# Optimization experiments

Measured on AMD Instinct MI355X. Metric: run time of the kernel, lower is better.

Reference implementation:

```python
import jax, jax.numpy as jnp
import numpy as np

T, D, FF, E, R = 4096, 1024, 2048, 4, 16
LORA_SCALE = 32.0 / 16.0  # alpha / r


def setup_inputs() -> dict:
    key = jax.random.key(0)
    ks = jax.random.split(key, 12)
    return {
        "x": jax.random.normal(ks[0], (T, D), jnp.float32),
        "gate_w": jax.random.normal(ks[1], (E, D), jnp.float32) * 0.03,
        "gate_up_w": jax.random.normal(ks[2], (D, 2 * FF), jnp.float32)[None].repeat(E, 0) * 0.0
                     + jax.random.normal(ks[2], (E, D, 2 * FF), jnp.float32) * 0.03,
        "gate_up_b": jax.random.normal(ks[3], (E, 2 * FF), jnp.float32) * 0.01,
        "down_w": jax.random.normal(ks[4], (E, FF, D), jnp.float32) * 0.02,
        "down_b": jax.random.normal(ks[5], (E, D), jnp.float32) * 0.01,
        "A_gate": jax.random.normal(ks[6], (E, R, D), jnp.float32) * 0.02,
        "B_gate": jax.random.normal(ks[7], (E, FF, R), jnp.float32) * 0.02,
        "A_up": jax.random.normal(ks[8], (E, R, D), jnp.float32) * 0.02,
        "B_up": jax.random.normal(ks[9], (E, FF, R), jnp.float32) * 0.02,
        "A_down": jax.random.normal(ks[10], (E, R, FF), jnp.float32) * 0.02,
        "B_down": jax.random.normal(ks[11], (E, D, R), jnp.float32) * 0.02,
        "top_k": 2,
    }


def reference(x, gate_w, gate_up_w, gate_up_b, down_w, down_b,
              A_gate, B_gate, A_up, B_up, A_down, B_down, top_k):
    t, d = x.shape
    e = gate_w.shape[0]
    # --- router: logits, softmax (fp32), top-k, renormalize ---
    router_logits = x @ gate_w.T                                   # [T,E]
    rw = jax.nn.softmax(router_logits.astype(jnp.float32), axis=1)
    top_w, sel = jax.lax.top_k(rw, top_k)                          # [T,k]
    top_w = top_w / jnp.sum(top_w, axis=-1, keepdims=True)
    top_w = top_w.astype(x.dtype)
    # dense per-token per-expert combine weights (scatter of top-k weights)
    w = jnp.zeros((t, e), x.dtype).at[jnp.arange(t)[:, None], sel].add(top_w)  # [T,E]
    # --- per-expert SwiGLU MLP with LoRA (vectorized over experts) ---
    gu = jnp.einsum('td,edf->etf', x, gate_up_w) + gate_up_b[:, None, :]       # [E,T,2FF]
    ff = gu.shape[-1] // 2
    gate = gu[..., :ff] + jnp.einsum('td,erd,efr->etf', x, A_gate, B_gate) * LORA_SCALE
    up = gu[..., ff:] + jnp.einsum('td,erd,efr->etf', x, A_up, B_up) * LORA_SCALE
    act = jax.nn.silu(gate) * up                                               # [E,T,FF]
    down = jnp.einsum('etf,efd->etd', act, down_w) + down_b[:, None, :]
    down = down + jnp.einsum('etf,erf,edr->etd', act, A_down, B_down) * LORA_SCALE
    # --- weighted scatter-combine ---
    final = jnp.einsum('etd,te->td', down, w)                                  # [T,D]
    return final, router_logits
```

## Files before the change

kernel.cpp:

```cpp
#include <hip/hip_runtime.h>

#define T_TOK 4096
#define DIM   1024
#define FFD   2048
#define NEXP  4
#define NRP   8704
#define MTILES 68

typedef unsigned short u16;
typedef __attribute__((ext_vector_type(8))) short short8;
typedef __attribute__((ext_vector_type(4))) float f32x4;
typedef __attribute__((ext_vector_type(8))) unsigned short u16x8;
typedef __attribute__((ext_vector_type(4))) unsigned short u16x4;

typedef __attribute__((address_space(1))) unsigned int as1_u32;
typedef __attribute__((address_space(3))) unsigned int as3_u32;

__device__ __forceinline__ u16 f2bf(float f) {
  union { float f; unsigned u; } v; v.f = f;
  unsigned u = v.u;
  return (u16)((u + 0x7fffu + ((u >> 16) & 1u)) >> 16);
}
__device__ __forceinline__ float bf2f(u16 h) {
  union { unsigned u; float f; } v; v.u = ((unsigned)h) << 16;
  return v.f;
}
__device__ __forceinline__ void gload16(const void* g, void* l) {
  __builtin_amdgcn_global_load_lds((const as1_u32*)g, (as3_u32*)l, 16, 0, 0);
}

__global__ void router_k(const float* __restrict__ x, const float* __restrict__ gw,
                         float* __restrict__ logits_out, int* __restrict__ sel,
                         float* __restrict__ selw) {
  int t = blockIdx.x;
  int lane = threadIdx.x;
  float xv[16];
#pragma unroll
  for (int i = 0; i < 16; ++i) xv[i] = x[(size_t)t * DIM + lane + i * 64];
  float l[4];
#pragma unroll
  for (int e = 0; e < 4; ++e) {
    float s = 0.f;
#pragma unroll
    for (int i = 0; i < 16; ++i) s += xv[i] * gw[e * DIM + lane + i * 64];
#pragma unroll
    for (int off = 32; off > 0; off >>= 1) s += __shfl_xor(s, off, 64);
    l[e] = s;
  }
  if (lane == 0) {
#pragma unroll
    for (int e = 0; e < 4; ++e) logits_out[(size_t)t * 4 + e] = l[e];
    int e0 = 0; float b0 = l[0];
    for (int e = 1; e < 4; ++e) if (l[e] > b0) { b0 = l[e]; e0 = e; }
    int e1 = -1; float b1 = -3.4e38f;
    for (int e = 0; e < 4; ++e) if (e != e0 && l[e] > b1) { b1 = l[e]; e1 = e; }
    float p1 = expf(b1 - b0);
    float w0 = 1.f / (1.f + p1);
    sel[2 * t] = e0; sel[2 * t + 1] = e1;
    selw[2 * t] = w0; selw[2 * t + 1] = 1.f - w0;
  }
}

__global__ void scan_k(const int* __restrict__ sel, int* __restrict__ pos,
                       int* __restrict__ offs, int* __restrict__ rowtok,
                       int* __restrict__ pairrow) {
  __shared__ int base[4];
  __shared__ int wsum[16][4];
  __shared__ int off_s[5];
  int tid = threadIdx.x, lane = tid & 63, wid = tid >> 6;
  if (tid < 4) base[tid] = 0;
  __syncthreads();
  for (int chunk = 0; chunk < 4; ++chunk) {
    int t = chunk * 1024 + tid;
    int e0 = sel[2 * t], e1 = sel[2 * t + 1];
    unsigned long long ltm = (1ull << lane) - 1ull;
    bool f[4]; int within[4];
#pragma unroll
    for (int e = 0; e < 4; ++e) {
      f[e] = (e0 == e) || (e1 == e);
      unsigned long long m = __ballot(f[e]);
      within[e] = __popcll(m & ltm);
      if (lane == 0) wsum[wid][e] = __popcll(m);
    }
    __syncthreads();
    int wbase[4] = {0, 0, 0, 0}, tot[4] = {0, 0, 0, 0};
    for (int i = 0; i < 16; ++i)
#pragma unroll
      for (int e = 0; e < 4; ++e) {
        int v = wsum[i][e];
        if (i < wid) wbase[e] += v;
        tot[e] += v;
      }
#pragma unroll
    for (int e = 0; e < 4; ++e)
      if (f[e]) {
        int p = base[e] + wbase[e] + within[e];
        if (e0 == e) pos[2 * t] = p; else pos[2 * t + 1] = p;
      }
    __syncthreads();
    if (tid < 4) base[tid] += tot[tid];
    __syncthreads();
  }
  if (tid == 0) {
    int o = 0;
    for (int e = 0; e < 4; ++e) { off_s[e] = o; o += ((base[e] + 127) >> 7) << 7; }
    off_s[4] = o;
    for (int i = 0; i < 5; ++i) offs[i] = off_s[i];
  }
  __syncthreads();
  for (int r = tid; r < NRP; r += 1024) rowtok[r] = -1;
  __syncthreads();
  for (int t = tid; t < T_TOK; t += 1024) {
#pragma unroll
    for (int s = 0; s < 2; ++s) {
      int e = sel[2 * t + s];
      int rr = off_s[e] + pos[2 * t + s];
      pairrow[2 * t + s] = rr;
      rowtok[rr] = t;
    }
  }
}

__global__ void gather_k(const float* __restrict__ x, const int* __restrict__ rowtok,
                         u16* __restrict__ xg) {
  int r = blockIdx.x, tid = threadIdx.x;
  int t = rowtok[r];
  float4 v = make_float4(0.f, 0.f, 0.f, 0.f);
  if (t >= 0) v = ((const float4*)(x + (size_t)t * DIM))[tid];
  u16x4 o;
  o[0] = f2bf(v.x); o[1] = f2bf(v.y); o[2] = f2bf(v.z); o[3] = f2bf(v.w);
  ((u16x4*)(xg + (size_t)r * DIM))[tid] = o;
}

__global__ void cvtA_k(const float* __restrict__ Ag, const float* __restrict__ Au,
                       const float* __restrict__ Ad, u16* __restrict__ abgu,
                       u16* __restrict__ adb) {
  int g = blockIdx.x * 256 + threadIdx.x;
  if (g < 32768) {
    int flat = g * 4;
    int e = flat >> 15;
    int rem = flat & 32767;
    int q = rem >> 10;
    int d = rem & 1023;
    const float* src = (q < 16) ? (Ag + ((size_t)e * 16 + q) * DIM + d)
                                : (Au + ((size_t)e * 16 + (q - 16)) * DIM + d);
    float4 v = *(const float4*)src;
    u16x4 o; o[0] = f2bf(v.x); o[1] = f2bf(v.y); o[2] = f2bf(v.z); o[3] = f2bf(v.w);
    *(u16x4*)(abgu + (size_t)flat) = o;
  } else {
    int flat = (g - 32768) * 4;
    float4 v = *(const float4*)(Ad + flat);
    u16x4 o; o[0] = f2bf(v.x); o[1] = f2bf(v.y); o[2] = f2bf(v.z); o[3] = f2bf(v.w);
    *(u16x4*)(adb + (size_t)flat) = o;
  }
}

__global__ void xa_k(const u16* __restrict__ xg, const u16* __restrict__ abgu,
                     const int* __restrict__ offs, float* __restrict__ xagu) {
  int r0 = blockIdx.x * 2, lane = threadIdx.x;
  int e = 0;
  if (r0 >= offs[1]) e = 1;
  if (r0 >= offs[2]) e = 2;
  if (r0 >= offs[3]) e = 3;
  float x0[16], x1[16];
#pragma unroll
  for (int i = 0; i < 4; ++i) {
    u16x4 v0 = ((const u16x4*)(xg + (size_t)r0 * DIM))[lane + i * 64];
    u16x4 v1 = ((const u16x4*)(xg + (size_t)(r0 + 1) * DIM))[lane + i * 64];
#pragma unroll
    for (int j = 0; j < 4; ++j) { x0[i * 4 + j] = bf2f(v0[j]); x1[i * 4 + j] = bf2f(v1[j]); }
  }
  const u16* A = abgu + (size_t)e * 32 * DIM;
  for (int q = 0; q < 32; ++q) {
    float s0 = 0.f, s1 = 0.f;
#pragma unroll
    for (int i = 0; i < 4; ++i) {
      u16x4 av = ((const u16x4*)(A + (size_t)q * DIM))[lane + i * 64];
#pragma unroll
      for (int j = 0; j < 4; ++j) {
        float a = bf2f(av[j]);
        s0 += x0[i * 4 + j] * a; s1 += x1[i * 4 + j] * a;
      }
    }
#pragma unroll
    for (int off = 32; off > 0; off >>= 1) { s0 += __shfl_xor(s0, off, 64); s1 += __shfl_xor(s1, off, 64); }
    if (lane == 0) { xagu[(size_t)r0 * 32 + q] = s0; xagu[(size_t)(r0 + 1) * 32 + q] = s1; }
  }
}

__global__ void aad_k(const u16* __restrict__ act, const u16* __restrict__ adb,
                      const int* __restrict__ offs, float* __restrict__ aad) {
  int r0 = blockIdx.x * 2, lane = threadIdx.x;
  int e = 0;
  if (r0 >= offs[1]) e = 1;
  if (r0 >= offs[2]) e = 2;
  if (r0 >= offs[3]) e = 3;
  float x0[32], x1[32];
#pragma unroll
  for (int i = 0; i < 8; ++i) {
    u16x4 v0 = ((const u16x4*)(act + (size_t)r0 * FFD))[lane + i * 64];
    u16x4 v1 = ((const u16x4*)(act + (size_t)(r0 + 1) * FFD))[lane + i * 64];
#pragma unroll
    for (int j = 0; j < 4; ++j) { x0[i * 4 + j] = bf2f(v0[j]); x1[i * 4 + j] = bf2f(v1[j]); }
  }
  const u16* A = adb + (size_t)e * 16 * FFD;
  for (int q = 0; q < 16; ++q) {
    float s0 = 0.f, s1 = 0.f;
#pragma unroll
    for (int i = 0; i < 8; ++i) {
      u16x4 av = ((const u16x4*)(A + (size_t)q * FFD))[lane + i * 64];
#pragma unroll
      for (int j = 0; j < 4; ++j) {
        float a = bf2f(av[j]);
        s0 += x0[i * 4 + j] * a; s1 += x1[i * 4 + j] * a;
      }
    }
#pragma unroll
    for (int off = 32; off > 0; off >>= 1) { s0 += __shfl_xor(s0, off, 64); s1 += __shfl_xor(s1, off, 64); }
    if (lane == 0) { aad[(size_t)r0 * 16 + q] = s0; aad[(size_t)(r0 + 1) * 16 + q] = s1; }
  }
}

__global__ void transpose_k(const float* __restrict__ in, u16* __restrict__ out,
                            int K, int N) {
  int e = blockIdx.z;
  int n0 = blockIdx.x * 32, k0 = blockIdx.y * 32;
  const float* I = in + (size_t)e * K * N;
  u16* O = out + (size_t)e * N * K;
  __shared__ u16 tile[32][33];
#pragma unroll
  for (int i = 0; i < 4; ++i) {
    int k = k0 + threadIdx.y + i * 8;
    tile[threadIdx.y + i * 8][threadIdx.x] = f2bf(I[(size_t)k * N + n0 + threadIdx.x]);
  }
  __syncthreads();
#pragma unroll
  for (int i = 0; i < 4; ++i) {
    int n = n0 + threadIdx.y + i * 8;
    O[(size_t)n * K + k0 + threadIdx.x] = tile[threadIdx.x][threadIdx.y + i * 8];
  }
}

__global__ __launch_bounds__(256, 2) void gemm1_k(
    const u16* __restrict__ xg, const u16* __restrict__ wgu_t,
    const float* __restrict__ gub, const float* __restrict__ Bg,
    const float* __restrict__ Bu, const float* __restrict__ xagu,
    const int* __restrict__ offs, u16* __restrict__ act) {
  __shared__ __align__(16) u16 sAB[36864];
  int tid = threadIdx.x, w = tid >> 6, lane = tid & 63;
  int f0 = blockIdx.x * 128;
  int row0 = blockIdx.y * 128;
  int e = 0;
  if (row0 >= offs[1]) e = 1;
  if (row0 >= offs[2]) e = 2;
  if (row0 >= offs[3]) e = 3;
  int wm = w >> 1, wn = w & 1;

  int srow = lane >> 2;
  int scol = ((lane & 3) ^ ((lane >> 3) & 3)) * 8;
  const u16* gA = xg + (size_t)(row0 + w * 32 + srow) * DIM + scol;
  int bhalf = (w < 2) ? (f0 + w * 64) : (2048 + f0 + (w - 2) * 64);
  const u16* gB = wgu_t + ((size_t)e << 22) + (size_t)(bhalf + srow) * DIM + scol;
  int fo = (((lane >> 4) ^ ((lane >> 1) & 3))) * 8;
  int arb = (wm * 64 + (lane & 15)) * 32 + fo;
  int brb = 4096 + (wn * 128 + (lane & 15)) * 32 + fo;

  f32x4 acc[4][8];
#pragma unroll
  for (int i = 0; i < 4; ++i)
#pragma unroll
    for (int j = 0; j < 8; ++j) acc[i][j] = f32x4{0.f, 0.f, 0.f, 0.f};

#pragma unroll
  for (int p = 0; p < 2; ++p) {
    u16* dA = sAB + p * 12288 + w * 1024;
    gload16(gA + p * 32, dA); gload16(gA + 16 * DIM + p * 32, dA + 512);
    u16* dB = sAB + p * 12288 + 4096 + w * 2048;
    gload16(gB + p * 32, dB); gload16(gB + 16 * DIM + p * 32, dB + 512);
    gload16(gB + 32 * DIM + p * 32, dB + 1024); gload16(gB + 48 * DIM + p * 32, dB + 1536);
  }
#pragma unroll
  for (int t = 0; t < 32; ++t) {
    if (t == 31) asm volatile("s_waitcnt vmcnt(0)\n\ts_barrier" ::: "memory");
    else         asm volatile("s_waitcnt vmcnt(6)\n\ts_barrier" ::: "memory");
    if (t < 30) {
      int kk = (t + 2) * 32;
      int bo = ((t + 2) % 3) * 12288;
      u16* dA = sAB + bo + w * 1024;
      gload16(gA + kk, dA); gload16(gA + 16 * DIM + kk, dA + 512);
      u16* dB = sAB + bo + 4096 + w * 2048;
      gload16(gB + kk, dB); gload16(gB + 16 * DIM + kk, dB + 512);
      gload16(gB + 32 * DIM + kk, dB + 1024); gload16(gB + 48 * DIM + kk, dB + 1536);
    }
    const u16* cb = sAB + (t % 3) * 12288;
    short8 a[4], bb[8];
#pragma unroll
    for (int mi = 0; mi < 4; ++mi)
      a[mi] = *(const short8*)&cb[arb + mi * 512];
#pragma unroll
    for (int ni = 0; ni < 8; ++ni)
      bb[ni] = *(const short8*)&cb[brb + ni * 512];
#pragma unroll
    for (int mi = 0; mi < 4; ++mi)
#pragma unroll
      for (int ni = 0; ni < 8; ++ni)
        acc[mi][ni] = __builtin_amdgcn_mfma_f32_16x16x32_bf16(a[mi], bb[ni], acc[mi][ni], 0, 0, 0);
  }

  __syncthreads();
  {
    int rl = tid & 127, half = tid >> 7;
    int sw = (rl >> 1) & 3;
    int abase = half * 12288 + rl * 32;
    u16 tmp[16];
#pragma unroll
    for (int q = 0; q < 16; ++q) tmp[q] = f2bf(2.f * xagu[(size_t)(row0 + rl) * 32 + half * 16 + q]);
    *(u16x8*)&sAB[abase + (0 ^ sw) * 8] = *(u16x8*)&tmp[0];
    *(u16x8*)&sAB[abase + (1 ^ sw) * 8] = *(u16x8*)&tmp[8];
    u16 t2[8] = {0x3f80, 0, 0, 0, 0, 0, 0, 0};
    u16 t3[8] = {0, 0, 0, 0, 0, 0, 0, 0};
    *(u16x8*)&sAB[abase + (2 ^ sw) * 8] = *(u16x8*)&t2[0];
    *(u16x8*)&sAB[abase + (3 ^ sw) * 8] = *(u16x8*)&t3[0];
    int r = tid, fb = r & 127, bh = r >> 7;
    int swb = (r >> 1) & 3;
    int bbase = 4096 + r * 32;
    const float* Bsrc = bh ? Bu : Bg;
    float bias = gub[e * 4096 + (bh ? (2048 + f0 + fb) : (f0 + fb))];
    u16 tb[16];
#pragma unroll
    for (int q = 0; q < 16; ++q) tb[q] = f2bf(Bsrc[((size_t)e * FFD + f0 + fb) * 16 + q]);
    *(u16x8*)&sAB[bbase + (0 ^ swb) * 8] = *(u16x8*)&tb[0];
    *(u16x8*)&sAB[bbase + (1 ^ swb) * 8] = *(u16x8*)&tb[8];
    u16 t2b[8] = {f2bf(bias), 0, 0, 0, 0, 0, 0, 0};
    *(u16x8*)&sAB[bbase + (2 ^ swb) * 8] = *(u16x8*)&t2b[0];
    *(u16x8*)&sAB[bbase + (3 ^ swb) * 8] = *(u16x8*)&t3[0];
  }
  __syncthreads();
  {
    int aBase = wn ? 12288 : 0;
    short8 a[4], bb[8];
#pragma unroll
    for (int mi = 0; mi < 4; ++mi)
      a[mi] = *(const short8*)&sAB[aBase + arb + mi * 512];
#pragma unroll
    for (int ni = 0; ni < 8; ++ni)
      bb[ni] = *(const short8*)&sAB[brb + ni * 512];
#pragma unroll
    for (int mi = 0; mi < 4; ++mi)
#pragma unroll
      for (int ni = 0; ni < 8; ++ni)
        acc[mi][ni] = __builtin_amdgcn_mfma_f32_16x16x32_bf16(a[mi], bb[ni], acc[mi][ni], 0, 0, 0);
  }
  __syncthreads();
#pragma unroll
  for (int mi = 0; mi < 4; ++mi)
#pragma unroll
    for (int ni = 0; ni < 8; ++ni)
#pragma unroll
      for (int j = 0; j < 4; ++j) {
        int row = wm * 64 + mi * 16 + (lane >> 4) * 4 + j;
        int br = wn * 128 + ni * 16 + (lane & 15);
        int key = ((row & 3) ^ ((row >> 2) & 3)) << 4;
        sAB[row * 256 + (br ^ key)] = f2bf(acc[mi][ni][j]);
      }
  __syncthreads();
  {
    int fc = (tid & 15) * 8;
    int rb = tid >> 4;
#pragma unroll
    for (int it = 0; it < 8; ++it) {
      int row = rb + it * 16;
      int key = ((row & 3) ^ ((row >> 2) & 3)) << 4;
      u16x8 gv = *(const u16x8*)&sAB[row * 256 + (fc ^ key)];
      u16x8 uv = *(const u16x8*)&sAB[row * 256 + 128 + (fc ^ key)];
      u16x8 ov;
#pragma unroll
      for (int j = 0; j < 8; ++j) {
        float g = bf2f(gv[j]);
        float u = bf2f(uv[j]);
        float s = g / (1.f + __expf(-g));
        ov[j] = f2bf(s * u);
      }
      *(u16x8*)(act + (size_t)(row0 + row) * FFD + f0 + fc) = ov;
    }
  }
}

__global__ __launch_bounds__(256, 2) void gemm2_k(
    const u16* __restrict__ act, const u16* __restrict__ wd_t,
    const float* __restrict__ db, const float* __restrict__ Bd,
    const float* __restrict__ aad, const int* __restrict__ offs,
    u16* __restrict__ down) {
  __shared__ __align__(16) u16 sAB[36864];
  int tid = threadIdx.x, w = tid >> 6, lane = tid & 63;
  int n0 = blockIdx.x * 256;
  int row0 = blockIdx.y * 128;
  int ks = blockIdx.z;
  size_t kbase = (size_t)ks * 1024;
  int e = 0;
  if (row0 >= offs[1]) e = 1;
  if (row0 >= offs[2]) e = 2;
  if (row0 >= offs[3]) e = 3;
  int wm = w >> 1, wn = w & 1;

  int srow = lane >> 2;
  int scol = ((lane & 3) ^ ((lane >> 3) & 3)) * 8;
  const u16* gA = act + (size_t)(row0 + w * 32 + srow) * FFD + kbase + scol;
  const u16* gB = wd_t + (size_t)e * DIM * FFD + (size_t)(n0 + w * 64 + srow) * FFD + kbase + scol;
  int fo = (((lane >> 4) ^ ((lane >> 1) & 3))) * 8;
  int arb = (wm * 64 + (lane & 15)) * 32 + fo;
  int brb = 4096 + (wn * 128 + (lane & 15)) * 32 + fo;

  f32x4 acc[4][8];
#pragma unroll
  for (int i = 0; i < 4; ++i)
#pragma unroll
    for (int j = 0; j < 8; ++j) acc[i][j] = f32x4{0.f, 0.f, 0.f, 0.f};

#pragma unroll
  for (int p = 0; p < 2; ++p) {
    u16* dA = sAB + p * 12288 + w * 1024;
    gload16(gA + p * 32, dA); gload16(gA + 16 * FFD + p * 32, dA + 512);
    u16* dB = sAB + p * 12288 + 4096 + w * 2048;
    gload16(gB + p * 32, dB); gload16(gB + 16 * FFD + p * 32, dB + 512);
    gload16(gB + 32 * FFD + p * 32, dB + 1024); gload16(gB + 48 * FFD + p * 32, dB + 1536);
  }
#pragma unroll
  for (int t = 0; t < 32; ++t) {
    if (t == 31) asm volatile("s_waitcnt vmcnt(0)\n\ts_barrier" ::: "memory");
    else         asm volatile("s_waitcnt vmcnt(6)\n\ts_barrier" ::: "memory");
    if (t < 30) {
      int kk = (t + 2) * 32;
      int bo = ((t + 2) % 3) * 12288;
      u16* dA = sAB + bo + w * 1024;
      gload16(gA + kk, dA); gload16(gA + 16 * FFD + kk, dA + 512);
      u16* dB = sAB + bo + 4096 + w * 2048;
      gload16(gB + kk, dB); gload16(gB + 16 * FFD + kk, dB + 512);
      gload16(gB + 32 * FFD + kk, dB + 1024); gload16(gB + 48 * FFD + kk, dB + 1536);
    }
    const u16* cb = sAB + (t % 3) * 12288;
    short8 a[4], bb[8];
#pragma unroll
    for (int mi = 0; mi < 4; ++mi)
      a[mi] = *(const short8*)&cb[arb + mi * 512];
#pragma unroll
    for (int ni = 0; ni < 8; ++ni)
      bb[ni] = *(const short8*)&cb[brb + ni * 512];
#pragma unroll
    for (int mi = 0; mi < 4; ++mi)
#pragma unroll
      for (int ni = 0; ni < 8; ++ni)
        acc[mi][ni] = __builtin_amdgcn_mfma_f32_16x16x32_bf16(a[mi], bb[ni], acc[mi][ni], 0, 0, 0);
  }

  if (ks == 0) {
    __syncthreads();
    {
      int r = tid >> 1, kh = tid & 1;
      int sw = (r >> 1) & 3;
      int o0 = r * 32 + ((2 * kh + 0) ^ sw) * 8;
      int o1 = r * 32 + ((2 * kh + 1) ^ sw) * 8;
      u16 tmp[16];
      if (kh == 0) {
#pragma unroll
        for (int q = 0; q < 16; ++q) tmp[q] = f2bf(2.f * aad[(size_t)(row0 + r) * 16 + q]);
      } else {
#pragma unroll
        for (int q = 0; q < 16; ++q) tmp[q] = 0;
        tmp[0] = 0x3f80;
      }
      *(u16x8*)&sAB[o0] = *(u16x8*)&tmp[0];
      *(u16x8*)&sAB[o1] = *(u16x8*)&tmp[8];
      int r2 = tid;
      int swb = (r2 >> 1) & 3;
      int bbase = 4096 + r2 * 32;
      u16 tb[16];
#pragma unroll
      for (int q = 0; q < 16; ++q) tb[q] = f2bf(Bd[((size_t)e * DIM + n0 + r2) * 16 + q]);
      *(u16x8*)&sAB[bbase + (0 ^ swb) * 8] = *(u16x8*)&tb[0];
      *(u16x8*)&sAB[bbase + (1 ^ swb) * 8] = *(u16x8*)&tb[8];
      u16 t2b[8] = {f2bf(db[e * DIM + n0 + r2]), 0, 0, 0, 0, 0, 0, 0};
      u16 t3b[8] = {0, 0, 0, 0, 0, 0, 0, 0};
      *(u16x8*)&sAB[bbase + (2 ^ swb) * 8] = *(u16x8*)&t2b[0];
      *(u16x8*)&sAB[bbase + (3 ^ swb) * 8] = *(u16x8*)&t3b[0];
    }
    __syncthreads();
    {
      short8 a[4], bb[8];
#pragma unroll
      for (int mi = 0; mi < 4; ++mi)
        a[mi] = *(const short8*)&sAB[arb + mi * 512];
#pragma unroll
      for (int ni = 0; ni < 8; ++ni)
        bb[ni] = *(const short8*)&sAB[brb + ni * 512];
#pragma unroll
      for (int mi = 0; mi < 4; ++mi)
#pragma unroll
        for (int ni = 0; ni < 8; ++ni)
          acc[mi][ni] = __builtin_amdgcn_mfma_f32_16x16x32_bf16(a[mi], bb[ni], acc[mi][ni], 0, 0, 0);
    }
  }
#pragma unroll
  for (int mi = 0; mi < 4; ++mi)
#pragma unroll
    for (int ni = 0; ni < 8; ++ni)
#pragma unroll
      for (int j = 0; j < 4; ++j) {
        int lr = wm * 64 + mi * 16 + (lane >> 4) * 4 + j;
        int lc = wn * 128 + ni * 16 + (lane & 15);
        down[((size_t)ks * NRP + row0 + lr) * DIM + n0 + lc] = f2bf(acc[mi][ni][j]);
      }
}

__global__ void combine_k(const u16* __restrict__ down, const int* __restrict__ pairrow,
                          const float* __restrict__ selw, float* __restrict__ out) {
  int t = blockIdx.x, tid = threadIdx.x;
  int r0 = pairrow[2 * t], r1 = pairrow[2 * t + 1];
  float w0 = selw[2 * t], w1 = selw[2 * t + 1];
  u16x4 a0 = *(const u16x4*)(down + ((size_t)r0) * DIM + tid * 4);
  u16x4 a1 = *(const u16x4*)(down + ((size_t)NRP + r0) * DIM + tid * 4);
  u16x4 b0 = *(const u16x4*)(down + ((size_t)r1) * DIM + tid * 4);
  u16x4 b1 = *(const u16x4*)(down + ((size_t)NRP + r1) * DIM + tid * 4);
  f32x4 o;
#pragma unroll
  for (int j = 0; j < 4; ++j)
    o[j] = w0 * (bf2f(a0[j]) + bf2f(a1[j])) + w1 * (bf2f(b0[j]) + bf2f(b1[j]));
  *(f32x4*)(out + (size_t)t * DIM + tid * 4) = o;
}

extern "C" void kernel_launch(void* const* d_in, const int* in_sizes, int n_in,
                              void* d_out, int out_size, void* d_ws, size_t ws_size,
                              hipStream_t stream) {
  const float* x         = (const float*)d_in[0];
  const float* gate_w    = (const float*)d_in[1];
  const float* gate_up_w = (const float*)d_in[2];
  const float* gate_up_b = (const float*)d_in[3];
  const float* down_w    = (const float*)d_in[4];
  const float* down_b    = (const float*)d_in[5];
  const float* A_gate    = (const float*)d_in[6];
  const float* B_gate    = (const float*)d_in[7];
  const float* A_up      = (const float*)d_in[8];
  const float* B_up      = (const float*)d_in[9];
  const float* A_down    = (const float*)d_in[10];
  const float* B_down    = (const float*)d_in[11];

  float* out_final  = (float*)d_out;
  float* out_logits = out_final + (size_t)T_TOK * DIM;

  char* ws = (char*)d_ws;
  size_t o = 0;
  auto take = [&](size_t bytes) -> void* {
    void* p = ws + o;
    o = (o + bytes + 255) & ~(size_t)255;
    return p;
  };
  int*   offs    = (int*)take(64);
  int*   sel     = (int*)take((size_t)T_TOK * 2 * 4);
  float* selw    = (float*)take((size_t)T_TOK * 2 * 4);
  int*   pos     = (int*)take((size_t)T_TOK * 2 * 4);
  int*   pairrow = (int*)take((size_t)T_TOK * 2 * 4);
  int*   rowtok  = (int*)take((size_t)NRP * 4);
  float* xagu    = (float*)take((size_t)NRP * 32 * 4);
  float* aadb    = (float*)take((size_t)NRP * 16 * 4);
  u16*   abgu    = (u16*)take((size_t)NEXP * 32 * DIM * 2);
  u16*   adb     = (u16*)take((size_t)NEXP * 16 * FFD * 2);
  u16*   xg      = (u16*)take((size_t)NRP * DIM * 2);
  u16*   actb    = (u16*)take((size_t)NRP * FFD * 2);
  u16*   downb   = (u16*)take((size_t)2 * NRP * DIM * 2);
  u16*   wgu_t   = (u16*)take((size_t)NEXP * 2 * FFD * DIM * 2);
  u16*   wd_t    = (u16*)take((size_t)NEXP * DIM * FFD * 2);
  (void)ws_size; (void)in_sizes; (void)n_in; (void)out_size;

  transpose_k<<<dim3(128, 32, NEXP), dim3(32, 8), 0, stream>>>(gate_up_w, wgu_t, DIM, 2 * FFD);
  transpose_k<<<dim3(32, 64, NEXP), dim3(32, 8), 0, stream>>>(down_w, wd_t, FFD, DIM);
  cvtA_k<<<256, 256, 0, stream>>>(A_gate, A_up, A_down, abgu, adb);

  router_k<<<T_TOK, 64, 0, stream>>>(x, gate_w, out_logits, sel, selw);
  scan_k<<<1, 1024, 0, stream>>>(sel, pos, offs, rowtok, pairrow);
  gather_k<<<NRP, 256, 0, stream>>>(x, rowtok, xg);
  xa_k<<<NRP / 2, 64, 0, stream>>>(xg, abgu, offs, xagu);
  gemm1_k<<<dim3(16, MTILES), 256, 0, stream>>>(xg, wgu_t, gate_up_b, B_gate, B_up,
                                                xagu, offs, actb);
  aad_k<<<NRP / 2, 64, 0, stream>>>(actb, adb, offs, aadb);
  gemm2_k<<<dim3(4, MTILES, 2), 256, 0, stream>>>(actb, wd_t, down_b, B_down, aadb, offs, downb);
  combine_k<<<T_TOK, 256, 0, stream>>>(downb, pairrow, selw, out_final);
}
```

Baseline: 260.0 us.

## Enlarge GEMM tiles to 256x256 with 512 threads and 4-stage pipeline

Both grouped GEMMs move from 128x256 tiles with 4 waves to 256x256 tiles with 8 waves. They now use a 4-buffer LDS ring with split A/B prefetch, interleaved MFMA halves, s_setprio and sched barriers. Per-expert row padding grows to multiples of 256, raising NRP to 9216. The larger tiles cut redundant global loads of weights and activations, at the cost of more padded rows, higher LDS use (128KB per block) and possible occupancy loss.

```diff
diff --git a/kernel.cpp b/kernel.cpp
--- a/kernel.cpp
+++ b/kernel.cpp
@@ -4,8 +4,7 @@
 #define DIM   1024
 #define FFD   2048
 #define NEXP  4
-#define NRP   8704
-#define MTILES 68
+#define NRP   9216
 
 typedef unsigned short u16;
 typedef __attribute__((ext_vector_type(8))) short short8;
@@ -103,7 +102,7 @@
   }
   if (tid == 0) {
     int o = 0;
-    for (int e = 0; e < 4; ++e) { off_s[e] = o; o += ((base[e] + 127) >> 7) << 7; }
+    for (int e = 0; e < 4; ++e) { off_s[e] = o; o += ((base[e] + 255) >> 8) << 8; }
     off_s[4] = o;
     for (int i = 0; i < 5; ++i) offs[i] = off_s[i];
   }
@@ -241,127 +240,148 @@
   }
 }
 
-__global__ __launch_bounds__(256, 2) void gemm1_k(
+__global__ __launch_bounds__(512, 2) void gemm1_k(
     const u16* __restrict__ xg, const u16* __restrict__ wgu_t,
     const float* __restrict__ gub, const float* __restrict__ Bg,
     const float* __restrict__ Bu, const float* __restrict__ xagu,
     const int* __restrict__ offs, u16* __restrict__ act) {
-  __shared__ __align__(16) u16 sAB[36864];
+  __shared__ __align__(16) u16 sAB[65536];
   int tid = threadIdx.x, w = tid >> 6, lane = tid & 63;
   int f0 = blockIdx.x * 128;
-  int row0 = blockIdx.y * 128;
+  int row0 = blockIdx.y * 256;
   int e = 0;
   if (row0 >= offs[1]) e = 1;
   if (row0 >= offs[2]) e = 2;
   if (row0 >= offs[3]) e = 3;
-  int wm = w >> 1, wn = w & 1;
-
-  int srow = lane >> 2;
+  int wm = w >> 2, wn = w & 3;
+
+  int srow = w * 16 + (lane >> 2);
   int scol = ((lane & 3) ^ ((lane >> 3) & 3)) * 8;
-  const u16* gA = xg + (size_t)(row0 + w * 32 + srow) * DIM + scol;
-  int bhalf = (w < 2) ? (f0 + w * 64) : (2048 + f0 + (w - 2) * 64);
-  const u16* gB = wgu_t + ((size_t)e << 22) + (size_t)(bhalf + srow) * DIM + scol;
-  int fo = (((lane >> 4) ^ ((lane >> 1) & 3))) * 8;
-  int arb = (wm * 64 + (lane & 15)) * 32 + fo;
-  int brb = 4096 + (wn * 128 + (lane & 15)) * 32 + fo;
-
-  f32x4 acc[4][8];
-#pragma unroll
-  for (int i = 0; i < 4; ++i)
-#pragma unroll
-    for (int j = 0; j < 8; ++j) acc[i][j] = f32x4{0.f, 0.f, 0.f, 0.f};
+  const u16* gA0 = xg + (size_t)(row0 + srow) * DIM + scol;
+  const u16* gA1 = gA0 + (size_t)128 * DIM;
+  const u16* gBg = wgu_t + ((size_t)e << 22) + (size_t)(f0 + srow) * DIM + scol;
+  const u16* gBu = wgu_t + ((size_t)e << 22) + (size_t)(2048 + f0 + srow) * DIM + scol;
+
+  int fo = ((lane >> 4) ^ ((lane >> 1) & 3)) * 8;
+  int ard = (wm * 128 + (lane & 15)) * 32 + fo;
+  int brd = 8192 + (wn * 64 + (lane & 15)) * 32 + fo;
+
+  f32x4 acc[8][4];
+#pragma unroll
+  for (int i = 0; i < 8; ++i)
+#pragma unroll
+    for (int j = 0; j < 4; ++j) acc[i][j] = f32x4{0.f, 0.f, 0.f, 0.f};
 
 #pragma unroll
   for (int p = 0; p < 2; ++p) {
-    u16* dA = sAB + p * 12288 + w * 1024;
-    gload16(gA + p * 32, dA); gload16(gA + 16 * DIM + p * 32, dA + 512);
-    u16* dB = sAB + p * 12288 + 4096 + w * 2048;
-    gload16(gB + p * 32, dB); gload16(gB + 16 * DIM + p * 32, dB + 512);
-    gload16(gB + 32 * DIM + p * 32, dB + 1024); gload16(gB + 48 * DIM + p * 32, dB + 1536);
-  }
-#pragma unroll
-  for (int t = 0; t < 32; ++t) {
-    if (t == 31) asm volatile("s_waitcnt vmcnt(0)\n\ts_barrier" ::: "memory");
-    else         asm volatile("s_waitcnt vmcnt(6)\n\ts_barrier" ::: "memory");
-    if (t < 30) {
-      int kk = (t + 2) * 32;
-      int bo = ((t + 2) % 3) * 12288;
-      u16* dA = sAB + bo + w * 1024;
-      gload16(gA + kk, dA); gload16(gA + 16 * DIM + kk, dA + 512);
-      u16* dB = sAB + bo + 4096 + w * 2048;
-      gload16(gB + kk, dB); gload16(gB + 16 * DIM + kk, dB + 512);
-      gload16(gB + 32 * DIM + kk, dB + 1024); gload16(gB + 48 * DIM + kk, dB + 1536);
-    }
-    const u16* cb = sAB + (t % 3) * 12288;
-    short8 a[4], bb[8];
-#pragma unroll
-    for (int mi = 0; mi < 4; ++mi)
-      a[mi] = *(const short8*)&cb[arb + mi * 512];
-#pragma unroll
-    for (int ni = 0; ni < 8; ++ni)
-      bb[ni] = *(const short8*)&cb[brb + ni * 512];
-#pragma unroll
-    for (int mi = 0; mi < 4; ++mi)
-#pragma unroll
-      for (int ni = 0; ni < 8; ++ni)
-        acc[mi][ni] = __builtin_amdgcn_mfma_f32_16x16x32_bf16(a[mi], bb[ni], acc[mi][ni], 0, 0, 0);
+    u16* s = sAB + p * 16384 + w * 512;
+    gload16(gA0 + p * 32, s);
+    gload16(gA1 + p * 32, s + 4096);
+    gload16(gBg + p * 32, s + 8192);
+    gload16(gBu + p * 32, s + 12288);
+  }
+
+#pragma unroll
+  for (int k = 0; k < 32; ++k) {
+    const u16* cb = sAB + (k & 3) * 16384;
+    if (k == 31) asm volatile("s_waitcnt vmcnt(0)" ::: "memory");
+    else         asm volatile("s_waitcnt vmcnt(4)" ::: "memory");
+    __builtin_amdgcn_s_barrier();
+    short8 a[4], b[4];
+#pragma unroll
+    for (int ni = 0; ni < 4; ++ni) b[ni] = *(const short8*)&cb[brd + ni * 512];
+#pragma unroll
+    for (int fr = 0; fr < 4; ++fr) a[fr] = *(const short8*)&cb[ard + fr * 512];
+    if (k + 2 < 32) {
+      u16* s = sAB + ((k + 2) & 3) * 16384 + w * 512;
+      gload16(gA0 + (k + 2) * 32, s);
+      gload16(gA1 + (k + 2) * 32, s + 4096);
+    }
+    asm volatile("s_waitcnt lgkmcnt(0)" ::: "memory");
+    __builtin_amdgcn_sched_barrier(0);
+    __builtin_amdgcn_s_setprio(1);
+#pragma unroll
+    for (int fr = 0; fr < 4; ++fr)
+#pragma unroll
+      for (int ni = 0; ni < 4; ++ni)
+        acc[fr][ni] = __builtin_amdgcn_mfma_f32_16x16x32_bf16(a[fr], b[ni], acc[fr][ni], 0, 0, 0);
+    __builtin_amdgcn_s_setprio(0);
+    __builtin_amdgcn_s_barrier();
+#pragma unroll
+    for (int fr = 0; fr < 4; ++fr) a[fr] = *(const short8*)&cb[ard + (fr + 4) * 512];
+    if (k + 2 < 32) {
+      u16* s = sAB + ((k + 2) & 3) * 16384 + w * 512;
+      gload16(gBg + (k + 2) * 32, s + 8192);
+      gload16(gBu + (k + 2) * 32, s + 12288);
+    }
+    asm volatile("s_waitcnt lgkmcnt(0)" ::: "memory");
+    __builtin_amdgcn_sched_barrier(0);
+    __builtin_amdgcn_s_setprio(1);
+#pragma unroll
+    for (int fr = 0; fr < 4; ++fr)
+#pragma unroll
+      for (int ni = 0; ni < 4; ++ni)
+        acc[fr + 4][ni] = __builtin_amdgcn_mfma_f32_16x16x32_bf16(a[fr], b[ni], acc[fr + 4][ni], 0, 0, 0);
+    __builtin_amdgcn_s_setprio(0);
+    __builtin_amdgcn_s_barrier();
   }
 
   __syncthreads();
   {
-    int rl = tid & 127, half = tid >> 7;
-    int sw = (rl >> 1) & 3;
-    int abase = half * 12288 + rl * 32;
+    int c = tid >> 8, r = tid & 255;
+    int key = (r >> 1) & 3;
+    u16* A = sAB + c * 16384 + r * 32;
     u16 tmp[16];
 #pragma unroll
-    for (int q = 0; q < 16; ++q) tmp[q] = f2bf(2.f * xagu[(size_t)(row0 + rl) * 32 + half * 16 + q]);
-    *(u16x8*)&sAB[abase + (0 ^ sw) * 8] = *(u16x8*)&tmp[0];
-    *(u16x8*)&sAB[abase + (1 ^ sw) * 8] = *(u16x8*)&tmp[8];
-    u16 t2[8] = {0x3f80, 0, 0, 0, 0, 0, 0, 0};
-    u16 t3[8] = {0, 0, 0, 0, 0, 0, 0, 0};
-    *(u16x8*)&sAB[abase + (2 ^ sw) * 8] = *(u16x8*)&t2[0];
-    *(u16x8*)&sAB[abase + (3 ^ sw) * 8] = *(u16x8*)&t3[0];
-    int r = tid, fb = r & 127, bh = r >> 7;
-    int swb = (r >> 1) & 3;
-    int bbase = 4096 + r * 32;
-    const float* Bsrc = bh ? Bu : Bg;
-    float bias = gub[e * 4096 + (bh ? (2048 + f0 + fb) : (f0 + fb))];
-    u16 tb[16];
-#pragma unroll
-    for (int q = 0; q < 16; ++q) tb[q] = f2bf(Bsrc[((size_t)e * FFD + f0 + fb) * 16 + q]);
-    *(u16x8*)&sAB[bbase + (0 ^ swb) * 8] = *(u16x8*)&tb[0];
-    *(u16x8*)&sAB[bbase + (1 ^ swb) * 8] = *(u16x8*)&tb[8];
-    u16 t2b[8] = {f2bf(bias), 0, 0, 0, 0, 0, 0, 0};
-    *(u16x8*)&sAB[bbase + (2 ^ swb) * 8] = *(u16x8*)&t2b[0];
-    *(u16x8*)&sAB[bbase + (3 ^ swb) * 8] = *(u16x8*)&t3[0];
+    for (int q = 0; q < 16; ++q) tmp[q] = f2bf(2.f * xagu[(size_t)(row0 + r) * 32 + c * 16 + q]);
+    u16 one8[8] = {0x3f80, 0, 0, 0, 0, 0, 0, 0};
+    u16 z8[8] = {0, 0, 0, 0, 0, 0, 0, 0};
+    *(u16x8*)&A[(0 ^ key) * 8] = *(u16x8*)&tmp[0];
+    *(u16x8*)&A[(1 ^ key) * 8] = *(u16x8*)&tmp[8];
+    *(u16x8*)&A[(2 ^ key) * 8] = *(u16x8*)&one8[0];
+    *(u16x8*)&A[(3 ^ key) * 8] = *(u16x8*)&z8[0];
+    if (tid < 256) {
+      int rb = tid;
+      int keyb = (rb >> 1) & 3;
+      u16* B = sAB + 8192 + rb * 32;
+      const float* Bsrc = (rb < 128) ? Bg : Bu;
+      int fb = (rb < 128) ? rb : (rb - 128);
+      float bias = gub[e * 4096 + ((rb < 128) ? (f0 + fb) : (2048 + f0 + fb))];
+      u16 tb[16];
+#pragma unroll
+      for (int q = 0; q < 16; ++q) tb[q] = f2bf(Bsrc[((size_t)e * FFD + f0 + fb) * 16 + q]);
+      u16 bb8[8] = {f2bf(bias), 0, 0, 0, 0, 0, 0, 0};
+      *(u16x8*)&B[(0 ^ keyb) * 8] = *(u16x8*)&tb[0];
+      *(u16x8*)&B[(1 ^ keyb) * 8] = *(u16x8*)&tb[8];
+      *(u16x8*)&B[(2 ^ keyb) * 8] = *(u16x8*)&bb8[0];
+      *(u16x8*)&B[(3 ^ keyb) * 8] = *(u16x8*)&z8[0];
+    }
   }
   __syncthreads();
   {
-    int aBase = wn ? 12288 : 0;
-    short8 a[4], bb[8];
-#pragma unroll
-    for (int mi = 0; mi < 4; ++mi)
-      a[mi] = *(const short8*)&sAB[aBase + arb + mi * 512];
-#pragma unroll
-    for (int ni = 0; ni < 8; ++ni)
-      bb[ni] = *(const short8*)&sAB[brb + ni * 512];
-#pragma unroll
-    for (int mi = 0; mi < 4; ++mi)
-#pragma unroll
-      for (int ni = 0; ni < 8; ++ni)
-        acc[mi][ni] = __builtin_amdgcn_mfma_f32_16x16x32_bf16(a[mi], bb[ni], acc[mi][ni], 0, 0, 0);
-  }
-  __syncthreads();
-#pragma unroll
-  for (int mi = 0; mi < 4; ++mi)
-#pragma unroll
-    for (int ni = 0; ni < 8; ++ni)
+    const u16* ca = sAB + (wn < 2 ? 0 : 16384);
+    short8 a[8], b[4];
+#pragma unroll
+    for (int ni = 0; ni < 4; ++ni) b[ni] = *(const short8*)&sAB[brd + ni * 512];
+#pragma unroll
+    for (int fr = 0; fr < 8; ++fr) a[fr] = *(const short8*)&ca[ard + fr * 512];
+#pragma unroll
+    for (int fr = 0; fr < 8; ++fr)
+#pragma unroll
+      for (int ni = 0; ni < 4; ++ni)
+        acc[fr][ni] = __builtin_amdgcn_mfma_f32_16x16x32_bf16(a[fr], b[ni], acc[fr][ni], 0, 0, 0);
+  }
+  __syncthreads();
+#pragma unroll
+  for (int fr = 0; fr < 8; ++fr)
+#pragma unroll
+    for (int ni = 0; ni < 4; ++ni)
 #pragma unroll
       for (int j = 0; j < 4; ++j) {
-        int row = wm * 64 + mi * 16 + (lane >> 4) * 4 + j;
-        int br = wn * 128 + ni * 16 + (lane & 15);
+        int row = wm * 128 + fr * 16 + (lane >> 4) * 4 + j;
+        int col = wn * 64 + ni * 16 + (lane & 15);
         int key = ((row & 3) ^ ((row >> 2) & 3)) << 4;
-        sAB[row * 256 + (br ^ key)] = f2bf(acc[mi][ni][j]);
+        sAB[row * 256 + (col ^ key)] = f2bf(acc[fr][ni][j]);
       }
   __syncthreads();
   {
@@ -369,10 +389,10 @@
     int rb = tid >> 4;
 #pragma unroll
     for (int it = 0; it < 8; ++it) {
-      int row = rb + it * 16;
+      int row = rb + it * 32;
       int key = ((row & 3) ^ ((row >> 2) & 3)) << 4;
       u16x8 gv = *(const u16x8*)&sAB[row * 256 + (fc ^ key)];
-      u16x8 uv = *(const u16x8*)&sAB[row * 256 + 128 + (fc ^ key)];
+      u16x8 uv = *(const u16x8*)&sAB[row * 256 + ((fc + 128) ^ key)];
       u16x8 ov;
 #pragma unroll
       for (int j = 0; j < 8; ++j) {
@@ -386,129 +406,142 @@
   }
 }
 
-__global__ __launch_bounds__(256, 2) void gemm2_k(
+__global__ __launch_bounds__(512, 2) void gemm2_k(
     const u16* __restrict__ act, const u16* __restrict__ wd_t,
     const float* __restrict__ db, const float* __restrict__ Bd,
     const float* __restrict__ aad, const int* __restrict__ offs,
     u16* __restrict__ down) {
-  __shared__ __align__(16) u16 sAB[36864];
+  __shared__ __align__(16) u16 sAB[65536];
   int tid = threadIdx.x, w = tid >> 6, lane = tid & 63;
   int n0 = blockIdx.x * 256;
-  int row0 = blockIdx.y * 128;
+  int row0 = blockIdx.y * 256;
   int ks = blockIdx.z;
   size_t kbase = (size_t)ks * 1024;
   int e = 0;
   if (row0 >= offs[1]) e = 1;
   if (row0 >= offs[2]) e = 2;
   if (row0 >= offs[3]) e = 3;
-  int wm = w >> 1, wn = w & 1;
-
-  int srow = lane >> 2;
+  int wm = w >> 2, wn = w & 3;
+
+  int srow = w * 16 + (lane >> 2);
   int scol = ((lane & 3) ^ ((lane >> 3) & 3)) * 8;
-  const u16* gA = act + (size_t)(row0 + w * 32 + srow) * FFD + kbase + scol;
-  const u16* gB = wd_t + (size_t)e * DIM * FFD + (size_t)(n0 + w * 64 + srow) * FFD + kbase + scol;
-  int fo = (((lane >> 4) ^ ((lane >> 1) & 3))) * 8;
-  int arb = (wm * 64 + (lane & 15)) * 32 + fo;
-  int brb = 4096 + (wn * 128 + (lane & 15)) * 32 + fo;
-
-  f32x4 acc[4][8];
-#pragma unroll
-  for (int i = 0; i < 4; ++i)
-#pragma unroll
-    for (int j = 0; j < 8; ++j) acc[i][j] = f32x4{0.f, 0.f, 0.f, 0.f};
+  const u16* gA0 = act + (size_t)(row0 + srow) * FFD + kbase + scol;
+  const u16* gA1 = gA0 + (size_t)128 * FFD;
+  const u16* gB0 = wd_t + (size_t)e * DIM * FFD + (size_t)(n0 + srow) * FFD + kbase + scol;
+  const u16* gB1 = gB0 + (size_t)128 * FFD;
+
+  int fo = ((lane >> 4) ^ ((lane >> 1) & 3)) * 8;
+  int ard = (wm * 128 + (lane & 15)) * 32 + fo;
+  int brd = 8192 + (wn * 64 + (lane & 15)) * 32 + fo;
+
+  f32x4 acc[8][4];
+#pragma unroll
+  for (int i = 0; i < 8; ++i)
+#pragma unroll
+    for (int j = 0; j < 4; ++j) acc[i][j] = f32x4{0.f, 0.f, 0.f, 0.f};
 
 #pragma unroll
   for (int p = 0; p < 2; ++p) {
-    u16* dA = sAB + p * 12288 + w * 1024;
-    gload16(gA + p * 32, dA); gload16(gA + 16 * FFD + p * 32, dA + 512);
-    u16* dB = sAB + p * 12288 + 4096 + w * 2048;
-    gload16(gB + p * 32, dB); gload16(gB + 16 * FFD + p * 32, dB + 512);
-    gload16(gB + 32 * FFD + p * 32, dB + 1024); gload16(gB + 48 * FFD + p * 32, dB + 1536);
-  }
-#pragma unroll
-  for (int t = 0; t < 32; ++t) {
-    if (t == 31) asm volatile("s_waitcnt vmcnt(0)\n\ts_barrier" ::: "memory");
-    else         asm volatile("s_waitcnt vmcnt(6)\n\ts_barrier" ::: "memory");
-    if (t < 30) {
-      int kk = (t + 2) * 32;
-      int bo = ((t + 2) % 3) * 12288;
-      u16* dA = sAB + bo + w * 1024;
-      gload16(gA + kk, dA); gload16(gA + 16 * FFD + kk, dA + 512);
-      u16* dB = sAB + bo + 4096 + w * 2048;
-      gload16(gB + kk, dB); gload16(gB + 16 * FFD + kk, dB + 512);
-      gload16(gB + 32 * FFD + kk, dB + 1024); gload16(gB + 48 * FFD + kk, dB + 1536);
-    }
-    const u16* cb = sAB + (t % 3) * 12288;
-    short8 a[4], bb[8];
-#pragma unroll
-    for (int mi = 0; mi < 4; ++mi)
-      a[mi] = *(const short8*)&cb[arb + mi * 512];
-#pragma unroll
-    for (int ni = 0; ni < 8; ++ni)
-      bb[ni] = *(const short8*)&cb[brb + ni * 512];
-#pragma unroll
-    for (int mi = 0; mi < 4; ++mi)
-#pragma unroll
-      for (int ni = 0; ni < 8; ++ni)
-        acc[mi][ni] = __builtin_amdgcn_mfma_f32_16x16x32_bf16(a[mi], bb[ni], acc[mi][ni], 0, 0, 0);
+    u16* s = sAB + p * 16384 + w * 512;
+    gload16(gA0 + p * 32, s);
+    gload16(gA1 + p * 32, s + 4096);
+    gload16(gB0 + p * 32, s + 8192);
+    gload16(gB1 + p * 32, s + 12288);
+  }
+
+#pragma unroll
+  for (int k = 0; k < 32; ++k) {
+    const u16* cb = sAB + (k & 3) * 16384;
+    if (k == 31) asm volatile("s_waitcnt vmcnt(0)" ::: "memory");
+    else         asm volatile("s_waitcnt vmcnt(4)" ::: "memory");
+    __builtin_amdgcn_s_barrier();
+    short8 a[4], b[4];
+#pragma unroll
+    for (int ni = 0; ni < 4; ++ni) b[ni] = *(const short8*)&cb[brd + ni * 512];
+#pragma unroll
+    for (int fr = 0; fr < 4; ++fr) a[fr] = *(const short8*)&cb[ard + fr * 512];
+    if (k + 2 < 32) {
+      u16* s = sAB + ((k + 2) & 3) * 16384 + w * 512;
+      gload16(gA0 + (k + 2) * 32, s);
+      gload16(gA1 + (k + 2) * 32, s + 4096);
+    }
+    asm volatile("s_waitcnt lgkmcnt(0)" ::: "memory");
+    __builtin_amdgcn_sched_barrier(0);
+    __builtin_amdgcn_s_setprio(1);
+#pragma unroll
+    for (int fr = 0; fr < 4; ++fr)
+#pragma unroll
+      for (int ni = 0; ni < 4; ++ni)
+        acc[fr][ni] = __builtin_amdgcn_mfma_f32_16x16x32_bf16(a[fr], b[ni], acc[fr][ni], 0, 0, 0);
+    __builtin_amdgcn_s_setprio(0);
+    __builtin_amdgcn_s_barrier();
+#pragma unroll
+    for (int fr = 0; fr < 4; ++fr) a[fr] = *(const short8*)&cb[ard + (fr + 4) * 512];
+    if (k + 2 < 32) {
+      u16* s = sAB + ((k + 2) & 3) * 16384 + w * 512;
+      gload16(gB0 + (k + 2) * 32, s + 8192);
+      gload16(gB1 + (k + 2) * 32, s + 12288);
+    }
+    asm volatile("s_waitcnt lgkmcnt(0)" ::: "memory");
+    __builtin_amdgcn_sched_barrier(0);
+    __builtin_amdgcn_s_setprio(1);
+#pragma unroll
+    for (int fr = 0; fr < 4; ++fr)
+#pragma unroll
+      for (int ni = 0; ni < 4; ++ni)
+        acc[fr + 4][ni] = __builtin_amdgcn_mfma_f32_16x16x32_bf16(a[fr], b[ni], acc[fr + 4][ni], 0, 0, 0);
+    __builtin_amdgcn_s_setprio(0);
+    __builtin_amdgcn_s_barrier();
   }
 
   if (ks == 0) {
     __syncthreads();
-    {
-      int r = tid >> 1, kh = tid & 1;
-      int sw = (r >> 1) & 3;
-      int o0 = r * 32 + ((2 * kh + 0) ^ sw) * 8;
-      int o1 = r * 32 + ((2 * kh + 1) ^ sw) * 8;
+    if (tid < 256) {
+      int r = tid;
+      int key = (r >> 1) & 3;
+      u16* A = sAB + r * 32;
       u16 tmp[16];
-      if (kh == 0) {
-#pragma unroll
-        for (int q = 0; q < 16; ++q) tmp[q] = f2bf(2.f * aad[(size_t)(row0 + r) * 16 + q]);
-      } else {
-#pragma unroll
-        for (int q = 0; q < 16; ++q) tmp[q] = 0;
-        tmp[0] = 0x3f80;
-      }
-      *(u16x8*)&sAB[o0] = *(u16x8*)&tmp[0];
-      *(u16x8*)&sAB[o1] = *(u16x8*)&tmp[8];
-      int r2 = tid;
-      int swb = (r2 >> 1) & 3;
-      int bbase = 4096 + r2 * 32;
+#pragma unroll
+      for (int q = 0; q < 16; ++q) tmp[q] = f2bf(2.f * aad[(size_t)(row0 + r) * 16 + q]);
+      u16 one8[8] = {0x3f80, 0, 0, 0, 0, 0, 0, 0};
+      u16 z8[8] = {0, 0, 0, 0, 0, 0, 0, 0};
+      *(u16x8*)&A[(0 ^ key) * 8] = *(u16x8*)&tmp[0];
+      *(u16x8*)&A[(1 ^ key) * 8] = *(u16x8*)&tmp[8];
+      *(u16x8*)&A[(2 ^ key) * 8] = *(u16x8*)&one8[0];
+      *(u16x8*)&A[(3 ^ key) * 8] = *(u16x8*)&z8[0];
+      u16* B = sAB + 8192 + r * 32;
       u16 tb[16];
 #pragma unroll
-      for (int q = 0; q < 16; ++q) tb[q] = f2bf(Bd[((size_t)e * DIM + n0 + r2) * 16 + q]);
-      *(u16x8*)&sAB[bbase + (0 ^ swb) * 8] = *(u16x8*)&tb[0];
-      *(u16x8*)&sAB[bbase + (1 ^ swb) * 8] = *(u16x8*)&tb[8];
-      u16 t2b[8] = {f2bf(db[e * DIM + n0 + r2]), 0, 0, 0, 0, 0, 0, 0};
-      u16 t3b[8] = {0, 0, 0, 0, 0, 0, 0, 0};
-      *(u16x8*)&sAB[bbase + (2 ^ swb) * 8] = *(u16x8*)&t2b[0];
-      *(u16x8*)&sAB[bbase + (3 ^ swb) * 8] = *(u16x8*)&t3b[0];
+      for (int q = 0; q < 16; ++q) tb[q] = f2bf(Bd[((size_t)e * DIM + n0 + r) * 16 + q]);
+      u16 bb8[8] = {f2bf(db[e * DIM + n0 + r]), 0, 0, 0, 0, 0, 0, 0};
+      *(u16x8*)&B[(0 ^ key) * 8] = *(u16x8*)&tb[0];
+      *(u16x8*)&B[(1 ^ key) * 8] = *(u16x8*)&tb[8];
+      *(u16x8*)&B[(2 ^ key) * 8] = *(u16x8*)&bb8[0];
+      *(u16x8*)&B[(3 ^ key) * 8] = *(u16x8*)&z8[0];
     }
     __syncthreads();
     {
-      short8 a[4], bb[8];
-#pragma unroll
-      for (int mi = 0; mi < 4; ++mi)
-        a[mi] = *(const short8*)&sAB[arb + mi * 512];
-#pragma unroll
-      for (int ni = 0; ni < 8; ++ni)
-        bb[ni] = *(const short8*)&sAB[brb + ni * 512];
-#pragma unroll
-      for (int mi = 0; mi < 4; ++mi)
-#pragma unroll
-        for (int ni = 0; ni < 8; ++ni)
-          acc[mi][ni] = __builtin_amdgcn_mfma_f32_16x16x32_bf16(a[mi], bb[ni], acc[mi][ni], 0, 0, 0);
-    }
-  }
-#pragma unroll
-  for (int mi = 0; mi < 4; ++mi)
-#pragma unroll
-    for (int ni = 0; ni < 8; ++ni)
+      short8 a[8], b[4];
+#pragma unroll
+      for (int ni = 0; ni < 4; ++ni) b[ni] = *(const short8*)&sAB[brd + ni * 512];
+#pragma unroll
+      for (int fr = 0; fr < 8; ++fr) a[fr] = *(const short8*)&sAB[ard + fr * 512];
+#pragma unroll
+      for (int fr = 0; fr < 8; ++fr)
+#pragma unroll
+        for (int ni = 0; ni < 4; ++ni)
+          acc[fr][ni] = __builtin_amdgcn_mfma_f32_16x16x32_bf16(a[fr], b[ni], acc[fr][ni], 0, 0, 0);
+    }
+  }
+#pragma unroll
+  for (int fr = 0; fr < 8; ++fr)
+#pragma unroll
+    for (int ni = 0; ni < 4; ++ni)
 #pragma unroll
       for (int j = 0; j < 4; ++j) {
-        int lr = wm * 64 + mi * 16 + (lane >> 4) * 4 + j;
-        int lc = wn * 128 + ni * 16 + (lane & 15);
-        down[((size_t)ks * NRP + row0 + lr) * DIM + n0 + lc] = f2bf(acc[mi][ni][j]);
+        int lr = wm * 128 + fr * 16 + (lane >> 4) * 4 + j;
+        int lc = wn * 64 + ni * 16 + (lane & 15);
+        down[((size_t)ks * NRP + row0 + lr) * DIM + n0 + lc] = f2bf(acc[fr][ni][j]);
       }
 }
 
@@ -579,9 +612,10 @@
   scan_k<<<1, 1024, 0, stream>>>(sel, pos, offs, rowtok, pairrow);
   gather_k<<<NRP, 256, 0, stream>>>(x, rowtok, xg);
   xa_k<<<NRP / 2, 64, 0, stream>>>(xg, abgu, offs, xagu);
-  gemm1_k<<<dim3(16, MTILES), 256, 0, stream>>>(xg, wgu_t, gate_up_b, B_gate, B_up,
-                                                xagu, offs, actb);
+  gemm1_k<<<dim3(16, NRP / 256), 512, 0, stream>>>(xg, wgu_t, gate_up_b, B_gate, B_up,
+                                                   xagu, offs, actb);
   aad_k<<<NRP / 2, 64, 0, stream>>>(actb, adb, offs, aadb);
-  gemm2_k<<<dim3(4, MTILES, 2), 256, 0, stream>>>(actb, wd_t, down_b, B_down, aadb, offs, downb);
+  gemm2_k<<<dim3(4, NRP / 256, 2), 512, 0, stream>>>(actb, wd_t, down_b, B_down, aadb,
+                                                     offs, downb);
   combine_k<<<T_TOK, 256, 0, stream>>>(downb, pairrow, selw, out_final);
 }
```

New measurement: 287.4 us. 10.5% more time.

## Software-pipeline LDS fragment loads with MFMA in both GEMM main loops

Applied to the files above, without the earlier changes.

Restructures the k-loop of both GEMM kernels so that LDS fragment reads for the next k-step are issued while MFMAs for the current step run. The B tile is split into two halves with setprio around the MFMA groups, and explicit lgkmcnt waits plus sched_barrier pin the ordering. The global prefetch wait tightens to vmcnt(0) each iteration and an extra barrier is added per iteration, which may add stalls. It also fixes the swizzle on the up-half read in the SwiGLU epilogue.

```diff
diff --git a/kernel.cpp b/kernel.cpp
--- a/kernel.cpp
+++ b/kernel.cpp
@@ -279,10 +279,22 @@
     gload16(gB + p * 32, dB); gload16(gB + 16 * DIM + p * 32, dB + 512);
     gload16(gB + 32 * DIM + p * 32, dB + 1024); gload16(gB + 48 * DIM + p * 32, dB + 1536);
   }
+  asm volatile("s_waitcnt vmcnt(6)" ::: "memory");
+  __builtin_amdgcn_s_barrier();
+  short8 aC[4], bL[4], bH[4], aN[4], bN[4];
+#pragma unroll
+  for (int fr = 0; fr < 4; ++fr) aC[fr] = *(const short8*)&sAB[arb + fr * 512];
+#pragma unroll
+  for (int ni = 0; ni < 4; ++ni) bL[ni] = *(const short8*)&sAB[brb + ni * 512];
+
 #pragma unroll
   for (int t = 0; t < 32; ++t) {
-    if (t == 31) asm volatile("s_waitcnt vmcnt(0)\n\ts_barrier" ::: "memory");
-    else         asm volatile("s_waitcnt vmcnt(6)\n\ts_barrier" ::: "memory");
+    const u16* cb  = sAB + (t % 3) * 12288;
+    const u16* cbn = sAB + ((t + 1) % 3) * 12288;
+#pragma unroll
+    for (int ni = 0; ni < 4; ++ni) bH[ni] = *(const short8*)&cb[brb + (ni + 4) * 512];
+    asm volatile("s_waitcnt vmcnt(0)" ::: "memory");
+    __builtin_amdgcn_s_barrier();
     if (t < 30) {
       int kk = (t + 2) * 32;
       int bo = ((t + 2) % 3) * 12288;
@@ -292,19 +304,38 @@
       gload16(gB + kk, dB); gload16(gB + 16 * DIM + kk, dB + 512);
       gload16(gB + 32 * DIM + kk, dB + 1024); gload16(gB + 48 * DIM + kk, dB + 1536);
     }
-    const u16* cb = sAB + (t % 3) * 12288;
-    short8 a[4], bb[8];
+    asm volatile("s_waitcnt lgkmcnt(4)" ::: "memory");
+    __builtin_amdgcn_sched_barrier(0);
+    __builtin_amdgcn_s_setprio(1);
 #pragma unroll
     for (int mi = 0; mi < 4; ++mi)
-      a[mi] = *(const short8*)&cb[arb + mi * 512];
-#pragma unroll
-    for (int ni = 0; ni < 8; ++ni)
-      bb[ni] = *(const short8*)&cb[brb + ni * 512];
+#pragma unroll
+      for (int ni = 0; ni < 4; ++ni)
+        acc[mi][ni] = __builtin_amdgcn_mfma_f32_16x16x32_bf16(aC[mi], bL[ni], acc[mi][ni], 0, 0, 0);
+    __builtin_amdgcn_s_setprio(0);
+    if (t < 31) {
+#pragma unroll
+      for (int fr = 0; fr < 4; ++fr) aN[fr] = *(const short8*)&cbn[arb + fr * 512];
+#pragma unroll
+      for (int ni = 0; ni < 4; ++ni) bN[ni] = *(const short8*)&cbn[brb + ni * 512];
+    }
+    __builtin_amdgcn_s_barrier();
+    if (t < 31) asm volatile("s_waitcnt lgkmcnt(8)" ::: "memory");
+    else        asm volatile("s_waitcnt lgkmcnt(0)" ::: "memory");
+    __builtin_amdgcn_sched_barrier(0);
+    __builtin_amdgcn_s_setprio(1);
 #pragma unroll
     for (int mi = 0; mi < 4; ++mi)
 #pragma unroll
-      for (int ni = 0; ni < 8; ++ni)
-        acc[mi][ni] = __builtin_amdgcn_mfma_f32_16x16x32_bf16(a[mi], bb[ni], acc[mi][ni], 0, 0, 0);
+      for (int ni = 0; ni < 4; ++ni)
+        acc[mi][ni + 4] = __builtin_amdgcn_mfma_f32_16x16x32_bf16(aC[mi], bH[ni], acc[mi][ni + 4], 0, 0, 0);
+    __builtin_amdgcn_s_setprio(0);
+    if (t < 31) {
+#pragma unroll
+      for (int fr = 0; fr < 4; ++fr) aC[fr] = aN[fr];
+#pragma unroll
+      for (int ni = 0; ni < 4; ++ni) bL[ni] = bN[ni];
+    }
   }
 
   __syncthreads();
@@ -372,7 +403,7 @@
       int row = rb + it * 16;
       int key = ((row & 3) ^ ((row >> 2) & 3)) << 4;
       u16x8 gv = *(const u16x8*)&sAB[row * 256 + (fc ^ key)];
-      u16x8 uv = *(const u16x8*)&sAB[row * 256 + 128 + (fc ^ key)];
+      u16x8 uv = *(const u16x8*)&sAB[row * 256 + ((fc + 128) ^ key)];
       u16x8 ov;
 #pragma unroll
       for (int j = 0; j < 8; ++j) {
@@ -425,10 +456,22 @@
     gload16(gB + p * 32, dB); gload16(gB + 16 * FFD + p * 32, dB + 512);
     gload16(gB + 32 * FFD + p * 32, dB + 1024); gload16(gB + 48 * FFD + p * 32, dB + 1536);
   }
+  asm volatile("s_waitcnt vmcnt(6)" ::: "memory");
+  __builtin_amdgcn_s_barrier();
+  short8 aC[4], bL[4], bH[4], aN[4], bN[4];
+#pragma unroll
+  for (int fr = 0; fr < 4; ++fr) aC[fr] = *(const short8*)&sAB[arb + fr * 512];
+#pragma unroll
+  for (int ni = 0; ni < 4; ++ni) bL[ni] = *(const short8*)&sAB[brb + ni * 512];
+
 #pragma unroll
   for (int t = 0; t < 32; ++t) {
-    if (t == 31) asm volatile("s_waitcnt vmcnt(0)\n\ts_barrier" ::: "memory");
-    else         asm volatile("s_waitcnt vmcnt(6)\n\ts_barrier" ::: "memory");
+    const u16* cb  = sAB + (t % 3) * 12288;
+    const u16* cbn = sAB + ((t + 1) % 3) * 12288;
+#pragma unroll
+    for (int ni = 0; ni < 4; ++ni) bH[ni] = *(const short8*)&cb[brb + (ni + 4) * 512];
+    asm volatile("s_waitcnt vmcnt(0)" ::: "memory");
+    __builtin_amdgcn_s_barrier();
     if (t < 30) {
       int kk = (t + 2) * 32;
       int bo = ((t + 2) % 3) * 12288;
@@ -438,19 +481,38 @@
       gload16(gB + kk, dB); gload16(gB + 16 * FFD + kk, dB + 512);
       gload16(gB + 32 * FFD + kk, dB + 1024); gload16(gB + 48 * FFD + kk, dB + 1536);
     }
-    const u16* cb = sAB + (t % 3) * 12288;
-    short8 a[4], bb[8];
+    asm volatile("s_waitcnt lgkmcnt(4)" ::: "memory");
+    __builtin_amdgcn_sched_barrier(0);
+    __builtin_amdgcn_s_setprio(1);
 #pragma unroll
     for (int mi = 0; mi < 4; ++mi)
-      a[mi] = *(const short8*)&cb[arb + mi * 512];
-#pragma unroll
-    for (int ni = 0; ni < 8; ++ni)
-      bb[ni] = *(const short8*)&cb[brb + ni * 512];
+#pragma unroll
+      for (int ni = 0; ni < 4; ++ni)
+        acc[mi][ni] = __builtin_amdgcn_mfma_f32_16x16x32_bf16(aC[mi], bL[ni], acc[mi][ni], 0, 0, 0);
+    __builtin_amdgcn_s_setprio(0);
+    if (t < 31) {
+#pragma unroll
+      for (int fr = 0; fr < 4; ++fr) aN[fr] = *(const short8*)&cbn[arb + fr * 512];
+#pragma unroll
+      for (int ni = 0; ni < 4; ++ni) bN[ni] = *(const short8*)&cbn[brb + ni * 512];
+    }
+    __builtin_amdgcn_s_barrier();
+    if (t < 31) asm volatile("s_waitcnt lgkmcnt(8)" ::: "memory");
+    else        asm volatile("s_waitcnt lgkmcnt(0)" ::: "memory");
+    __builtin_amdgcn_sched_barrier(0);
+    __builtin_amdgcn_s_setprio(1);
 #pragma unroll
     for (int mi = 0; mi < 4; ++mi)
 #pragma unroll
-      for (int ni = 0; ni < 8; ++ni)
-        acc[mi][ni] = __builtin_amdgcn_mfma_f32_16x16x32_bf16(a[mi], bb[ni], acc[mi][ni], 0, 0, 0);
+      for (int ni = 0; ni < 4; ++ni)
+        acc[mi][ni + 4] = __builtin_amdgcn_mfma_f32_16x16x32_bf16(aC[mi], bH[ni], acc[mi][ni + 4], 0, 0, 0);
+    __builtin_amdgcn_s_setprio(0);
+    if (t < 31) {
+#pragma unroll
+      for (int fr = 0; fr < 4; ++fr) aC[fr] = aN[fr];
+#pragma unroll
+      for (int ni = 0; ni < 4; ++ni) bL[ni] = bN[ni];
+    }
   }
 
   if (ks == 0) {
```

Measured after the change: 272.1 us. 1.05x slower.
